# Kernel tuning notes

Measured on AMD Instinct MI355X. Metric: run time of the kernel, lower is better.

Reference implementation:

```python
import jax, jax.numpy as jnp
import numpy as np

DIM = 512
H = 8
HEAD = DIM // H
SCALE = HEAD ** -0.5
B, XL, KL = 4, 1024, 256


def _split(t):
    b, n, _ = t.shape
    return t.reshape(b, n, H, HEAD).transpose(0, 2, 1, 3)


def _merge(t):
    b, h, n, d = t.shape
    return t.transpose(0, 2, 1, 3).reshape(b, n, h * d)


def _qkv(t, W):
    q, k, v = jnp.split(t @ W, 3, axis=-1)
    return _split(q), _split(k), _split(v)


def setup_inputs() -> dict:
    key = jax.random.key(0)
    ks = jax.random.split(key, 20)
    def n(i, shape):
        return jax.random.normal(ks[i], shape, dtype=jnp.float32)
    return {
        "x": n(0, (B, XL, DIM)),
        "kernal": n(1, (B, KL, DIM)),
        "i_x": n(2, (B, XL, DIM)),
        "i_kernal": n(3, (B, KL, DIM)),
        "rd": jax.random.randint(ks[4], (B, KL, XL), 0, 66),
        "polar_pos": jax.random.randint(ks[5], (B, KL, XL), 0, 8),
        "att_mask": jax.random.bernoulli(ks[6], 0.1, (B, H, XL, KL)),
        "i_att_mask": jax.random.bernoulli(ks[7], 0.1, (B, H, XL, KL)),
        "cross_att_mask": jax.random.bernoulli(ks[8], 0.1, (B, H, XL, KL)),
        "Wqkv": n(9, (DIM, 3 * DIM)) * 0.02,
        "Wqkv_i": n(10, (DIM, 3 * DIM)) * 0.02,
        "Wqkv_i2": n(11, (DIM, 3 * DIM)) * 0.02,
        "Wproj": n(12, (DIM, DIM)) * 0.02,
        "bproj": jnp.zeros((DIM,), jnp.float32),
        "Wproj_i": n(13, (DIM, DIM)) * 0.02,
        "bproj_i": jnp.zeros((DIM,), jnp.float32),
        "Wproj_i2": n(14, (DIM, DIM)) * 0.02,
        "bproj_i2": jnp.zeros((DIM,), jnp.float32),
        "dis_embed": n(15, (66, H)) * 0.02,
        "polar_emb": n(16, (8, 1)) * 0.02,
    }


def reference(x, kernal, i_x, i_kernal, rd, polar_pos, att_mask, i_att_mask, cross_att_mask, Wqkv, Wqkv_i, Wqkv_i2, Wproj, bproj, Wproj_i, bproj_i, Wproj_i2, bproj_i2, dis_embed, polar_emb):
    q, k, v = _qkv(x, Wqkv)
    k_q, k_k, k_v = _qkv(kernal, Wqkv)
    i_q, i_k, i_v = _qkv(i_x, Wqkv_i)
    i_k_q, i_k_k, i_k_v = _qkv(i_kernal, Wqkv_i)

    rd_bias = dis_embed[rd].transpose(0, 3, 1, 2)              # [b,h,kl,xl]
    k_x_attn = jnp.einsum('bhkd,bhxd->bhkx', k_q, k) * SCALE   # [b,h,kl,xl]

    # main-orientation: per (b,h,k) sum of |attn| over x grouped by polar bin
    polar = jnp.clip(polar_pos, 0, 7)[:, None, :, :]           # [b,1,kl,xl]
    abs_attn = jnp.abs(k_x_attn)
    ori_sum = jnp.stack([jnp.sum(abs_attn * (polar == o), axis=-1) for o in range(8)], axis=-1)  # [b,h,kl,8]
    main_ori = jnp.argmax(ori_sum, axis=-1)                    # [b,h,kl]
    new_polar = polar - main_ori[..., None]
    new_polar = jnp.where(new_polar < 0, new_polar + 8, new_polar)
    polar_bias = polar_emb[new_polar, 0]                       # [b,h,kl,xl]

    kx = jnp.where(jnp.transpose(att_mask, (0, 1, 3, 2)), -1e6, k_x_attn)
    kx = jax.nn.softmax(kx + rd_bias + polar_bias, axis=-1)
    k_out = _merge(jnp.einsum('bhkx,bhxd->bhkd', kx, v)) @ Wproj + bproj

    x_k = jnp.einsum('bhxd,bhkd->bhxk', q, k_k) * SCALE
    x_k = jnp.where(att_mask, -1e9, x_k)
    x_k = jax.nn.softmax(x_k + jnp.transpose(rd_bias + polar_bias, (0, 1, 3, 2)), axis=-1)
    x_out1 = _merge(jnp.einsum('bhxk,bhkd->bhxd', x_k, k_v)) @ Wproj + bproj

    x_ik = jnp.einsum('bhxd,bhkd->bhxk', q, i_k_k) * SCALE
    x_ik = jax.nn.softmax(jnp.where(cross_att_mask, -1e9, x_ik), axis=-1)
    x_out2 = _merge(jnp.einsum('bhxk,bhkd->bhxd', x_ik, i_k_v)) @ Wproj + bproj
    x_out = x_out1 + x_out2

    ik_ix = jnp.einsum('bhkd,bhxd->bhkx', i_k_q, i_k) * SCALE
    ik_ix = jnp.where(jnp.transpose(i_att_mask, (0, 1, 3, 2)), -1e9, ik_ix)
    ik_ix = jax.nn.softmax(ik_ix, axis=-1)
    i_k_out = _merge(jnp.einsum('bhkx,bhxd->bhkd', ik_ix, i_v)) @ Wproj_i + bproj_i

    i_k2_q, i_k2_k, i_k2_v = _qkv(i_k_out, Wqkv_i2)
    ix_ik2 = jnp.einsum('bhxd,bhkd->bhxk', i_q, i_k2_k) * SCALE
    ix_ik2 = jax.nn.softmax(jnp.where(i_att_mask, -1e9, ix_ik2), axis=-1)
    i_x_out = _merge(jnp.einsum('bhxk,bhkd->bhxd', ix_ik2, i_k2_v)) @ Wproj_i2 + bproj_i2

    return (x_out, k_out, i_x_out)
```

## Files before the change

### kernel.cpp

```cpp
#include <hip/hip_runtime.h>
#include <cstddef>
#include <cstdint>

#define BB 4
#define HH 8
#define HEADD 64
#define DIMM 512
#define XLL 1024
#define KLL 256
#define BHH (BB*HH)

typedef __attribute__((ext_vector_type(8))) short bf16x8;
typedef __attribute__((ext_vector_type(8))) unsigned short u16x8;
typedef __attribute__((ext_vector_type(4))) float f32x4;
typedef unsigned short u16;

__device__ __forceinline__ u16 f2b(float f) {
    unsigned int u = __builtin_bit_cast(unsigned int, f);
    u = u + 0x7fffu + ((u >> 16) & 1u);
    return (u16)(u >> 16);
}
__device__ __forceinline__ float b2f(u16 h) {
    unsigned int u = ((unsigned int)h) << 16;
    return __builtin_bit_cast(float, u);
}
__device__ __forceinline__ f32x4 mfma16(bf16x8 a, bf16x8 b, f32x4 c) {
    return __builtin_amdgcn_mfma_f32_16x16x32_bf16(a, b, c, 0, 0, 0);
}
__device__ __forceinline__ float wred_max(float v) {
    #pragma unroll
    for (int o = 1; o < 64; o <<= 1) v = fmaxf(v, __shfl_xor(v, o, 64));
    return v;
}
__device__ __forceinline__ float wred_sum(float v) {
    #pragma unroll
    for (int o = 1; o < 64; o <<= 1) v += __shfl_xor(v, o, 64);
    return v;
}


__global__ __launch_bounds__(256) void prep_all_k(
    const float* __restrict__ s0, const float* __restrict__ s1,
    const float* __restrict__ s2, const float* __restrict__ s3,
    const float* __restrict__ s4, const float* __restrict__ s5,
    u16* __restrict__ d0, u16* __restrict__ d1, u16* __restrict__ d2,
    u16* __restrict__ d3, u16* __restrict__ d4, u16* __restrict__ d5,
    const int* __restrict__ i_att, unsigned char* __restrict__ iattT8,
    u16* __restrict__ iattBF,
    const int* __restrict__ cross, u16* __restrict__ crossBF)
{
    const int id = blockIdx.x;
    if (id < 3072) {
        __shared__ float t[32][33];
        const float* W; u16* Wt; int N, bx, by;
        if (id < 2304) {
            int which = id / 768, local = id - which * 768;
            W = which == 0 ? s0 : (which == 1 ? s1 : s2);
            Wt = which == 0 ? d0 : (which == 1 ? d1 : d2);
            N = 1536; bx = local % 48; by = local / 48;
        } else {
            int which = (id - 2304) / 256, local = (id - 2304) % 256;
            W = which == 0 ? s3 : (which == 1 ? s4 : s5);
            Wt = which == 0 ? d3 : (which == 1 ? d4 : d5);
            N = 512; bx = local % 16; by = local / 16;
        }
        const int K = 512;
        int tx = threadIdx.x & 31, ty = threadIdx.x >> 5;
        #pragma unroll
        for (int r = ty; r < 32; r += 8)
            t[r][tx] = W[(size_t)(by * 32 + r) * N + bx * 32 + tx];
        __syncthreads();
        #pragma unroll
        for (int r = ty; r < 32; r += 8)
            Wt[(size_t)(bx * 32 + r) * K + by * 32 + tx] = f2b(t[tx][r]);
        return;
    }
    const int id2 = id - 3072;
    const int xt = id2 & 31, kt = (id2 >> 5) & 7, z = id2 >> 8;
    const int bh = z & 31;
    const int tid = threadIdx.x;
    const u16 NEG = f2b(-1e9f);
    const int sl = tid >> 7, rem = tid & 127, l = rem >> 1, nilow = rem & 1;
    const int lg = l >> 4, lr_ = l & 15;
    const int xl0 = sl * 16 + lg * 4, kl = nilow * 16 + lr_;
    if (z < 32) {
        __shared__ unsigned char t8[32][33];
        const int tx = tid & 31, ty = tid >> 5;
        #pragma unroll
        for (int r = ty; r < 32; r += 8)
            t8[r][tx] = (unsigned char)(i_att[((size_t)bh * 1024 + xt * 32 + r) * 256 + kt * 32 + tx] != 0);
        __syncthreads();
        #pragma unroll
        for (int r = ty; r < 32; r += 8)
            iattT8[((size_t)bh * 256 + kt * 32 + r) * 1024 + xt * 32 + tx] = t8[tx][r];
        ushort4 o;
        o.x = t8[xl0 + 0][kl] ? NEG : (u16)0;
        o.y = t8[xl0 + 1][kl] ? NEG : (u16)0;
        o.z = t8[xl0 + 2][kl] ? NEG : (u16)0;
        o.w = t8[xl0 + 3][kl] ? NEG : (u16)0;
        size_t eb = (((size_t)bh * 64 + xt * 2 + sl) * 8 + kt) * 512 + (size_t)l * 8 + nilow * 4;
        *reinterpret_cast<ushort4*>(iattBF + eb) = o;
    } else {
        const int kg = kt * 32 + kl;
        u16 o_[4];
        #pragma unroll
        for (int j = 0; j < 4; ++j) {
            int mm = cross[((size_t)bh * 1024 + xt * 32 + xl0 + j) * 256 + kg];
            o_[j] = mm ? NEG : (u16)0;
        }
        ushort4 o; o.x = o_[0]; o.y = o_[1]; o.z = o_[2]; o.w = o_[3];
        size_t eb = (((size_t)bh * 64 + xt * 2 + sl) * 8 + kt) * 512 + (size_t)l * 8 + nilow * 4;
        *reinterpret_cast<ushort4*>(crossBF + eb) = o;
    }
}

__global__ __launch_bounds__(256) void main_ori_k8(
    const u16* __restrict__ S, const int* __restrict__ polar,
    int* __restrict__ MO)
{
    const int blk = blockIdx.x;
    const int b = blk >> 8, k = blk & 255;
    const int tid = threadIdx.x;
    const int wave = tid >> 6, lane = tid & 63;
    const int c = tid * 4;
    int4 p4 = *reinterpret_cast<const int4*>(polar + ((size_t)b * 256 + k) * 1024 + c);
    int pp[4] = { p4.x, p4.y, p4.z, p4.w };
    #pragma unroll
    for (int j = 0; j < 4; ++j) { int p = pp[j]; pp[j] = p < 0 ? 0 : (p > 7 ? 7 : p); }
    __shared__ float sred[4][8];
    for (int h = 0; h < 8; ++h) {
        const int bh = b * 8 + h;
        ushort4 sv = *reinterpret_cast<const ushort4*>(S + ((size_t)bh * 256 + k) * 1024 + c);
        float av[4] = { fabsf(b2f(sv.x)), fabsf(b2f(sv.y)), fabsf(b2f(sv.z)), fabsf(b2f(sv.w)) };
        float bins[8] = {};
        #pragma unroll
        for (int j = 0; j < 4; ++j) {
            #pragma unroll
            for (int o = 0; o < 8; ++o) bins[o] += (pp[j] == o) ? av[j] : 0.0f;
        }
        #pragma unroll
        for (int o = 0; o < 8; ++o) bins[o] = wred_sum(bins[o]);
        if (lane == 0) {
            #pragma unroll
            for (int o = 0; o < 8; ++o) sred[wave][o] = bins[o];
        }
        __syncthreads();
        if (tid == 0) {
            int best = 0; float bv = -1.0f;
            #pragma unroll
            for (int o = 0; o < 8; ++o) {
                float s = sred[0][o] + sred[1][o] + sred[2][o] + sred[3][o];
                if (s > bv) { bv = s; best = o; }
            }
            MO[bh * 256 + k] = best;
        }
        __syncthreads();
    }
}

__global__ __launch_bounds__(256) void bias_build_k(
    const int* __restrict__ rd, const int* __restrict__ polar,
    const int* __restrict__ att, const float* __restrict__ dis,
    const float* __restrict__ pemb, const int* __restrict__ MO,
    u16* __restrict__ biasF, u16* __restrict__ bias1)
{
    const int b = blockIdx.z;
    const int xt = blockIdx.x * 32, kt = blockIdx.y * 32;
    const int tid = threadIdx.x;
    __shared__ float dsh[528];
    __shared__ int rds[32][33];
    __shared__ int pls[32][33];
    __shared__ u16 bt[32][33];
    for (int i = tid; i < 528; i += 256) dsh[i] = dis[i];
    const int tx = tid & 31, ty = tid >> 5;
    #pragma unroll
    for (int r = ty; r < 32; r += 8) {
        size_t src = ((size_t)b * 256 + kt + r) * 1024 + xt + tx;
        rds[tx][r] = rd[src];
        int p = polar[src]; pls[tx][r] = p < 0 ? 0 : (p > 7 ? 7 : p);
    }
    float pe[8];
    #pragma unroll
    for (int o = 0; o < 8; ++o) pe[o] = pemb[o];
    __syncthreads();
    const int sl = tid >> 7, rem = tid & 127, l = rem >> 1, nilow = rem & 1;
    const int lg = l >> 4, lr_ = l & 15;
    const int xl0 = sl * 16 + lg * 4, kl = nilow * 16 + lr_;
    const int kg = kt + kl;
    const u16 NEG9 = f2b(-1e9f), NEG6 = f2b(-1e6f);
    for (int h = 0; h < 8; ++h) {
        const int bh = b * 8 + h;
        int mo = MO[bh * 256 + kg];
        u16 o9[4];
        #pragma unroll
        for (int j = 0; j < 4; ++j) {
            int xl = xl0 + j;
            int mm = att[((size_t)bh * 1024 + xt + xl) * 256 + kg];
            float v = dsh[rds[xl][kl] * 8 + h] + pe[(pls[xl][kl] - mo + 8) & 7];
            u16 vb = f2b(v);
            o9[j] = mm ? NEG9 : vb;
            bt[xl][kl] = mm ? NEG6 : vb;
        }
        size_t eb = (((size_t)bh * 64 + (xt >> 4) + sl) * 8 + (kt >> 5)) * 512 + (size_t)l * 8 + nilow * 4;
        ushort4 ov; ov.x = o9[0]; ov.y = o9[1]; ov.z = o9[2]; ov.w = o9[3];
        *reinterpret_cast<ushort4*>(biasF + eb) = ov;
        __syncthreads();
        const int k_ = tid >> 3, x4 = (tid & 7) * 4;
        ushort4 o2;
        o2.x = bt[x4 + 0][k_]; o2.y = bt[x4 + 1][k_];
        o2.z = bt[x4 + 2][k_]; o2.w = bt[x4 + 3][k_];
        *reinterpret_cast<ushort4*>(bias1 + ((size_t)bh * 256 + kt + k_) * 1024 + xt + x4) = o2;
        __syncthreads();
    }
}

template<typename AT>
__device__ __forceinline__ void gemm_core_128(
    const AT* __restrict__ A, const AT* __restrict__ A2,
    const u16* __restrict__ Wt,
    int rb, int cb, short* Asl, short* Bsl, f32x4 (&acc)[4][4])
{
    constexpr bool F32 = sizeof(AT) == 4;
    const int tid = threadIdx.x;
    const int w = tid >> 6, lane = tid & 63;
    const int lr = lane & 15, lk = (lane >> 4) * 8;
    const int wr = (w >> 1) * 64, wc = (w & 1) * 64;
    const int srow = tid >> 3, skc = (tid & 7) * 8;
    const AT* gA = A + (size_t)(rb + srow) * 512 + skc;
    const AT* gA2 = A2 ? A2 + (size_t)(rb + srow) * 512 + skc : nullptr;
    const u16* gB = Wt + (size_t)(cb + srow) * 512 + skc;
    float4 ral[4], rah[4];
    bf16x8 rab[4], rab2[4], rw[4];
    #pragma unroll
    for (int it = 0; it < 4; ++it) {
        if constexpr (F32) {
            ral[it] = *reinterpret_cast<const float4*>(gA + (size_t)it * 32 * 512);
            rah[it] = *reinterpret_cast<const float4*>(gA + (size_t)it * 32 * 512 + 4);
        } else {
            rab[it] = *reinterpret_cast<const bf16x8*>(gA + (size_t)it * 32 * 512);
            if (gA2) rab2[it] = *reinterpret_cast<const bf16x8*>(gA2 + (size_t)it * 32 * 512);
        }
        rw[it] = *reinterpret_cast<const bf16x8*>(gB + (size_t)it * 32 * 512);
    }
    for (int t = 0; t < 8; ++t) {
        #pragma unroll
        for (int it = 0; it < 4; ++it) {
            if constexpr (F32) {
                u16x8 o;
                o[0] = f2b(ral[it].x); o[1] = f2b(ral[it].y);
                o[2] = f2b(ral[it].z); o[3] = f2b(ral[it].w);
                o[4] = f2b(rah[it].x); o[5] = f2b(rah[it].y);
                o[6] = f2b(rah[it].z); o[7] = f2b(rah[it].w);
                *reinterpret_cast<u16x8*>(&Asl[(it * 32 + srow) * 72 + skc]) = o;
            } else {
                if (gA2) {
                    u16x8 o;
                    #pragma unroll
                    for (int e = 0; e < 8; ++e)
                        o[e] = f2b(b2f((u16)rab[it][e]) + b2f((u16)rab2[it][e]));
                    *reinterpret_cast<u16x8*>(&Asl[(it * 32 + srow) * 72 + skc]) = o;
                } else {
                    *reinterpret_cast<bf16x8*>(&Asl[(it * 32 + srow) * 72 + skc]) = rab[it];
                }
            }
            *reinterpret_cast<bf16x8*>(&Bsl[(it * 32 + srow) * 72 + skc]) = rw[it];
        }
        if (t < 7) {
            const int k0 = (t + 1) * 64;
            #pragma unroll
            for (int it = 0; it < 4; ++it) {
                if constexpr (F32) {
                    ral[it] = *reinterpret_cast<const float4*>(gA + k0 + (size_t)it * 32 * 512);
                    rah[it] = *reinterpret_cast<const float4*>(gA + k0 + (size_t)it * 32 * 512 + 4);
                } else {
                    rab[it] = *reinterpret_cast<const bf16x8*>(gA + k0 + (size_t)it * 32 * 512);
                    if (gA2) rab2[it] = *reinterpret_cast<const bf16x8*>(gA2 + k0 + (size_t)it * 32 * 512);
                }
                rw[it] = *reinterpret_cast<const bf16x8*>(gB + k0 + (size_t)it * 32 * 512);
            }
        }
        __syncthreads();
        #pragma unroll
        for (int ks = 0; ks < 2; ++ks) {
            bf16x8 af[4], bf_[4];
            #pragma unroll
            for (int mi = 0; mi < 4; ++mi)
                af[mi] = *reinterpret_cast<const bf16x8*>(&Asl[(wr + mi * 16 + lr) * 72 + ks * 32 + lk]);
            #pragma unroll
            for (int ni = 0; ni < 4; ++ni)
                bf_[ni] = *reinterpret_cast<const bf16x8*>(&Bsl[(wc + ni * 16 + lr) * 72 + ks * 32 + lk]);
            #pragma unroll
            for (int mi = 0; mi < 4; ++mi)
                #pragma unroll
                for (int ni = 0; ni < 4; ++ni)
                    acc[mi][ni] = mfma16(af[mi], bf_[ni], acc[mi][ni]);
        }
        __syncthreads();
    }
}

template<typename AT>
__device__ __forceinline__ void qkv_body(
    const AT* __restrict__ A, const u16* __restrict__ Wt,
    u16* __restrict__ qb, u16* __restrict__ kb, u16* __restrict__ vt,
    int sl, int rb, int cb)
{
    __shared__ __align__(16) short Ls[2 * 128 * 72];
    short* Asl = Ls;
    short* Bsl = Ls + 128 * 72;
    f32x4 acc[4][4] = {};
    gemm_core_128<AT>(A, nullptr, Wt, rb, cb, Asl, Bsl, acc);
    const int tid = threadIdx.x;
    const int wave = tid >> 6, lane = tid & 63;
    const int lr = lane & 15, lg = lane >> 4;
    const int wr = (wave >> 1) * 64, wc = (wave & 1) * 64;
    const int seq = 1 << sl, smask = seq - 1;
    if (cb < 1024) {
        const float scl = (cb < 512) ? 0.125f : 1.0f;
        #pragma unroll
        for (int mi = 0; mi < 4; ++mi)
            #pragma unroll
            for (int ni = 0; ni < 4; ++ni) {
                int row = wr + mi * 16 + lg * 4;
                int col = wc + ni * 16 + lr;
                f32x4 v = acc[mi][ni];
                #pragma unroll
                for (int j = 0; j < 4; ++j)
                    Ls[(row + j) * 136 + col] = (short)f2b(v[j] * scl);
            }
        __syncthreads();
        u16* dst = (cb < 512) ? qb : kb;
        if (dst) {
            const int cbase = (cb < 512) ? cb : cb - 512;
            #pragma unroll
            for (int p = 0; p < 8; ++p) {
                int slot = p * 256 + tid;
                int row = slot >> 4;
                int half = (slot >> 3) & 1;
                int inner = slot & 7;
                int m = rb + row;
                int bb = m >> sl, n = m & smask;
                int cg = cbase + half * 64;
                int h = cg >> 6;
                u16x8 val = *reinterpret_cast<u16x8*>(&Ls[row * 136 + half * 64 + inner * 8]);
                *reinterpret_cast<u16x8*>(
                    &dst[(((size_t)bb * HH + h) * seq + n) * 64 + inner * 8]) = val;
            }
        }
    } else {
        #pragma unroll
        for (int mi = 0; mi < 4; ++mi)
            #pragma unroll
            for (int ni = 0; ni < 4; ++ni) {
                int col = wc + ni * 16 + lr;
                int row0 = wr + mi * 16 + lg * 4;
                f32x4 v = acc[mi][ni];
                #pragma unroll
                for (int j = 0; j < 4; ++j)
                    Ls[col * 136 + row0 + j] = (short)f2b(v[j]);
            }
        __syncthreads();
        const int bb = rb >> sl, n0 = rb & smask;
        #pragma unroll
        for (int p = 0; p < 4; ++p) {
            int slot = p * 256 + tid;
            int col = slot >> 3;
            int inner = slot & 7;
            int dg = (cb - 1024) + col;
            int h = dg >> 6, d = dg & 63;
            u16* vrow = vt + ((((size_t)bb * HH + h) * 64 + d) << sl) + n0;
            u16x8 v0 = *reinterpret_cast<u16x8*>(&Ls[col * 136 + inner * 8]);
            u16x8 v1 = *reinterpret_cast<u16x8*>(&Ls[col * 136 + 64 + inner * 8]);
            *reinterpret_cast<u16x8*>(vrow + inner * 8) = v0;
            *reinterpret_cast<u16x8*>(vrow + 64 + inner * 8) = v1;
        }
    }
}

__global__ __launch_bounds__(256, 3) void gemm_qkv_all_k(
    const float* __restrict__ A0, const float* __restrict__ A1,
    const float* __restrict__ A2, const float* __restrict__ A3,
    const u16* __restrict__ W01, const u16* __restrict__ W23,
    u16* q0, u16* k0, u16* v0, u16* q1, u16* k1, u16* v1,
    u16* q2, u16* k2, u16* v2, u16* q3, u16* k3, u16* v3)
{
    const int lin = blockIdx.x;
    const int swz = (lin & 7) * 120 + (lin >> 3);
    const int x = swz % 12, y = swz / 12;
    const float* A; const u16* Wt; u16 *qb, *kb, *vt; int sl, ry;
    if (y < 32)      { A = A0; Wt = W01; qb = q0; kb = k0; vt = v0; sl = 10; ry = y; }
    else if (y < 40) { A = A1; Wt = W01; qb = q1; kb = k1; vt = v1; sl = 8;  ry = y - 32; }
    else if (y < 72) { A = A2; Wt = W23; qb = q2; kb = k2; vt = v2; sl = 10; ry = y - 40; }
    else             { A = A3; Wt = W23; qb = q3; kb = k3; vt = v3; sl = 8;  ry = y - 72; }
    qkv_body<float>(A, Wt, qb, kb, vt, sl, ry * 128, x * 128);
}

__global__ __launch_bounds__(256, 3) void gemm_qkv2_k(
    const u16* __restrict__ A, const u16* __restrict__ Wt,
    u16* kb, u16* vt)
{
    qkv_body<u16>(A, Wt, nullptr, kb, vt, 8, blockIdx.y * 128, (blockIdx.x + 4) * 128);
}

template<bool OUTBF>
__device__ __forceinline__ void proj_body(
    const u16* __restrict__ A, const u16* __restrict__ A2,
    const u16* __restrict__ Wt,
    const float* __restrict__ bias, float bscale, void* __restrict__ outp,
    int rb, int cb)
{
    __shared__ __align__(16) short Ls[2 * 128 * 72];
    f32x4 acc[4][4] = {};
    gemm_core_128<u16>(A, A2, Wt, rb, cb, Ls, Ls + 128 * 72, acc);
    const int tid = threadIdx.x;
    const int wave = tid >> 6, lane = tid & 63;
    const int lr = lane & 15;
    const int wr = (wave >> 1) * 64, wc = (wave & 1) * 64;
    #pragma unroll
    for (int mi = 0; mi < 4; ++mi) {
        int m0 = rb + wr + mi * 16 + (lane >> 4) * 4;
        #pragma unroll
        for (int ni = 0; ni < 4; ++ni) {
            int c = cb + wc + ni * 16 + lr;
            float bv = bscale * bias[c];
            f32x4 v = acc[mi][ni];
            #pragma unroll
            for (int j = 0; j < 4; ++j) {
                size_t o = (size_t)(m0 + j) * 512 + c;
                if (OUTBF) reinterpret_cast<u16*>(outp)[o] = f2b(v[j] + bv);
                else       reinterpret_cast<float*>(outp)[o] = v[j] + bv;
            }
        }
    }
}

__global__ __launch_bounds__(256, 3) void gemm_proj_bf16_k(
    const u16* __restrict__ A, const u16* __restrict__ Wt,
    const float* __restrict__ bias, float bscale, u16* __restrict__ outp)
{
    proj_body<true>(A, nullptr, Wt, bias, bscale, outp, blockIdx.y * 128, blockIdx.x * 128);
}

__global__ __launch_bounds__(256, 3) void gemm_proj3_k(
    const u16* __restrict__ A0, const u16* __restrict__ A0b,
    const u16* __restrict__ A1, const u16* __restrict__ A2,
    const u16* __restrict__ W, const u16* __restrict__ Wi2,
    const float* __restrict__ bp, const float* __restrict__ bpi2,
    float* __restrict__ o0, float* __restrict__ o1, float* __restrict__ o2)
{
    const int id = blockIdx.x;
    const u16 *A, *Ax; const u16* Wt; const float* bias; float bscale; float* outp; int x, y;
    if (id < 128)      { A = A0; Ax = A0b; Wt = W;   bias = bp;   bscale = 2.0f; outp = o0; x = id & 3; y = id >> 2; }
    else if (id < 256) { A = A1; Ax = nullptr; Wt = Wi2; bias = bpi2; bscale = 1.0f; outp = o1; x = (id - 128) & 3; y = (id - 128) >> 2; }
    else               { A = A2; Ax = nullptr; Wt = W;   bias = bp;   bscale = 1.0f; outp = o2; x = (id - 256) & 3; y = (id - 256) >> 2; }
    proj_body<false>(A, Ax, Wt, bias, bscale, outp, y * 128, x * 128);
}

__global__ __launch_bounds__(256, 4) void scores_pair_k(
    const u16* __restrict__ A1, const u16* __restrict__ B1, u16* __restrict__ S1,
    const u16* __restrict__ A2, const u16* __restrict__ B2, u16* __restrict__ S2)
{
    __shared__ __align__(16) short Ls[2 * 128 * 72];
    short* As = Ls;
    short* Bs = Ls + 128 * 72;
    const int z = blockIdx.z, bh = z & 31;
    const u16* Aq = (z < 32) ? A1 : A2;
    const u16* Bk = (z < 32) ? B1 : B2;
    u16* S = (z < 32) ? S1 : S2;
    const int tid = threadIdx.x;
    const int wave = tid >> 6, lane = tid & 63;
    const int lr = lane & 15, lg = lane >> 4, lk = lg * 8;
    const int rb = blockIdx.y * 128, cb = blockIdx.x * 128;
    const int wr = (wave >> 1) * 64, wc = (wave & 1) * 64;
    const u16* Ap = Aq + (size_t)bh * 256 * 64;
    const u16* Bp = Bk + (size_t)bh * 1024 * 64;
    const int srow = tid >> 3, skc = (tid & 7) * 8;
    #pragma unroll
    for (int it = 0; it < 4; ++it) {
        int row = it * 32 + srow;
        *reinterpret_cast<bf16x8*>(&As[row * 72 + skc]) =
            *reinterpret_cast<const bf16x8*>(Ap + (size_t)(rb + row) * 64 + skc);
        *reinterpret_cast<bf16x8*>(&Bs[row * 72 + skc]) =
            *reinterpret_cast<const bf16x8*>(Bp + (size_t)(cb + row) * 64 + skc);
    }
    __syncthreads();
    f32x4 acc[4][4] = {};
    #pragma unroll
    for (int ks = 0; ks < 2; ++ks) {
        bf16x8 af[4], bf_[4];
        #pragma unroll
        for (int mi = 0; mi < 4; ++mi)
            af[mi] = *reinterpret_cast<const bf16x8*>(&As[(wr + mi * 16 + lr) * 72 + ks * 32 + lk]);
        #pragma unroll
        for (int ni = 0; ni < 4; ++ni)
            bf_[ni] = *reinterpret_cast<const bf16x8*>(&Bs[(wc + ni * 16 + lr) * 72 + ks * 32 + lk]);
        #pragma unroll
        for (int mi = 0; mi < 4; ++mi)
            #pragma unroll
            for (int ni = 0; ni < 4; ++ni)
                acc[mi][ni] = mfma16(af[mi], bf_[ni], acc[mi][ni]);
    }
    __syncthreads();
    #pragma unroll
    for (int mi = 0; mi < 4; ++mi)
        #pragma unroll
        for (int ni = 0; ni < 4; ++ni) {
            int row = wr + mi * 16 + lg * 4;
            int col = wc + ni * 16 + lr;
            f32x4 v = acc[mi][ni];
            #pragma unroll
            for (int j = 0; j < 4; ++j)
                Ls[(row + j) * 136 + col] = (short)f2b(v[j]);
        }
    __syncthreads();
    #pragma unroll
    for (int p = 0; p < 8; ++p) {
        int slot = p * 256 + tid;
        int row = slot >> 4;
        int chunk = slot & 15;
        u16x8 val = *reinterpret_cast<u16x8*>(&Ls[row * 136 + chunk * 8]);
        *reinterpret_cast<u16x8*>(
            &S[((size_t)bh * 256 + rb + row) * 1024 + cb + chunk * 8]) = val;
    }
}

__global__ __launch_bounds__(256) void softmax_pair_k(
    u16* __restrict__ S1, const u16* __restrict__ bias1,
    u16* __restrict__ S2, const unsigned char* __restrict__ maskT)
{
    const int rg = blockIdx.x;
    const bool first = rg < 8192;
    const int row_g = first ? rg : rg - 8192;
    const int tid = threadIdx.x;
    const int wave = tid >> 6, lane = tid & 63;
    const int c = tid * 4;
    u16* rowp = (first ? S1 : S2) + (size_t)row_g * 1024;
    ushort4 sv = *reinterpret_cast<const ushort4*>(rowp + c);
    float s[4] = { b2f(sv.x), b2f(sv.y), b2f(sv.z), b2f(sv.w) };
    if (first) {
        ushort4 bv = *reinterpret_cast<const ushort4*>(bias1 + (size_t)row_g * 1024 + c);
        s[0] += b2f(bv.x); s[1] += b2f(bv.y); s[2] += b2f(bv.z); s[3] += b2f(bv.w);
    } else {
        uchar4 mk = *reinterpret_cast<const uchar4*>(maskT + (size_t)row_g * 1024 + c);
        if (mk.x) s[0] = -1e9f; if (mk.y) s[1] = -1e9f;
        if (mk.z) s[2] = -1e9f; if (mk.w) s[3] = -1e9f;
    }
    __shared__ float swv[4];
    float lm = fmaxf(fmaxf(s[0], s[1]), fmaxf(s[2], s[3]));
    lm = wred_max(lm);
    if (lane == 0) swv[wave] = lm;
    __syncthreads();
    float m = fmaxf(fmaxf(swv[0], swv[1]), fmaxf(swv[2], swv[3]));
    __syncthreads();
    float ls = 0.0f;
    #pragma unroll
    for (int j = 0; j < 4; ++j) { s[j] = __expf(s[j] - m); ls += s[j]; }
    ls = wred_sum(ls);
    if (lane == 0) swv[wave] = ls;
    __syncthreads();
    float inv = 1.0f / (swv[0] + swv[1] + swv[2] + swv[3]);
    ushort4 ov = { f2b(s[0] * inv), f2b(s[1] * inv), f2b(s[2] * inv), f2b(s[3] * inv) };
    *reinterpret_cast<ushort4*>(rowp + c) = ov;
}

__global__ __launch_bounds__(256, 4) void pv_pair_k(
    const u16* __restrict__ P1, const u16* __restrict__ V1, u16* __restrict__ o1,
    const u16* __restrict__ P2, const u16* __restrict__ V2, u16* __restrict__ o2)
{
    __shared__ __align__(16) short Ps[4 * 16 * 72];
    const int z = blockIdx.z;
    const u16* P = z ? P2 : P1;
    const u16* V = z ? V2 : V1;
    u16* out = z ? o2 : o1;
    const int tid = threadIdx.x;
    const int wave = tid >> 6, lane = tid & 63;
    const int lr = lane & 15, lg = lane >> 4, lk = lg * 8;
    const int bh = blockIdx.y, b = bh >> 3, h = bh & 7;
    const int rb = blockIdx.x * 64;
    const int wr = wave * 16;
    f32x4 acc[4] = {};
    const u16* Pb = P + ((size_t)bh * 256 + rb) * 1024;
    const u16* Vb = V + (size_t)bh * 64 * 1024;
    for (int c0 = 0; c0 < 1024; c0 += 64) {
        #pragma unroll
        for (int ks = 0; ks < 2; ++ks) {
            bf16x8 ap = *reinterpret_cast<const bf16x8*>(
                Pb + (size_t)(wr + lr) * 1024 + c0 + ks * 32 + lk);
            #pragma unroll
            for (int ni = 0; ni < 4; ++ni) {
                bf16x8 vv = *reinterpret_cast<const bf16x8*>(
                    Vb + (size_t)(ni * 16 + lr) * 1024 + c0 + ks * 32 + lk);
                acc[ni] = mfma16(ap, vv, acc[ni]);
            }
        }
    }
    short* myP = &Ps[wave * 16 * 72];
    #pragma unroll
    for (int ni = 0; ni < 4; ++ni) {
        int d = ni * 16 + lr;
        f32x4 v = acc[ni];
        #pragma unroll
        for (int j = 0; j < 4; ++j)
            myP[(lg * 4 + j) * 72 + d] = (short)f2b(v[j]);
    }
    #pragma unroll
    for (int p = 0; p < 2; ++p) {
        int slot = p * 64 + lane;
        int rloc = slot >> 3;
        int inner = slot & 7;
        int r0 = rb + wr + rloc;
        u16x8 val = *reinterpret_cast<u16x8*>(&myP[rloc * 72 + inner * 8]);
        *reinterpret_cast<u16x8*>(
            &out[((size_t)(b * 256 + r0)) * 512 + h * 64 + inner * 8]) = val;
    }
}

__global__ __launch_bounds__(256, 4) void attn_all_k(
    const u16* __restrict__ Q0, const u16* __restrict__ IQ0,
    const u16* __restrict__ K1, const u16* __restrict__ V1t,
    const u16* __restrict__ B1F, u16* __restrict__ out1,
    const u16* __restrict__ K2, const u16* __restrict__ V2t,
    const u16* __restrict__ B2F, u16* __restrict__ out2,
    const u16* __restrict__ K3, const u16* __restrict__ V3t,
    const u16* __restrict__ B3F, u16* __restrict__ out3)
{
    const int tid = threadIdx.x;
    const int w = tid >> 6, lane = tid & 63;
    const int lr = lane & 15, lg = lane >> 4, lk = lg * 8;
    int lin = blockIdx.x;
    const u16 *Qp, *Kp, *Vp, *BF; u16* outm;
    if (lin < 512)        { Qp = Q0;  Kp = K1; Vp = V1t; BF = B1F; outm = out1; }
    else if (lin < 1024)  { Qp = Q0;  Kp = K2; Vp = V2t; BF = B2F; outm = out2; lin -= 512; }
    else                  { Qp = IQ0; Kp = K3; Vp = V3t; BF = B3F; outm = out3; lin -= 1024; }
    const int xcd = lin & 7, idx = lin >> 3;
    const int bh = xcd * 4 + (idx & 3);
    const int rb = (idx >> 2) * 64;
    const int b = bh >> 3, h = bh & 7;
    const int wr = w * 16;
    const int strip = (rb >> 4) + w;

    __shared__ __align__(16) short Ps[4 * 16 * 264];
    short* myP = &Ps[w * 16 * 264];

    bf16x8 qf0, qf1;
    {
        const u16* Qb = Qp + ((size_t)bh * 1024 + rb + wr + lr) * 64;
        qf0 = *reinterpret_cast<const bf16x8*>(Qb + lk);
        qf1 = *reinterpret_cast<const bf16x8*>(Qb + 32 + lk);
    }

    bf16x8 breg[8];
    {
        const u16* bb = BF + (((size_t)bh * 64 + strip) * 8) * 512 + (size_t)lane * 8;
        #pragma unroll
        for (int itp = 0; itp < 8; ++itp)
            breg[itp] = *reinterpret_cast<const bf16x8*>(bb + (size_t)itp * 512);
    }
    const u16* Kb = Kp + (size_t)bh * 256 * 64;
    f32x4 acc[16];
    #pragma unroll
    for (int ni = 0; ni < 16; ++ni) acc[ni] = (f32x4){0.f, 0.f, 0.f, 0.f};
    #pragma unroll
    for (int ni = 0; ni < 16; ++ni) {
        bf16x8 b0 = *reinterpret_cast<const bf16x8*>(Kb + (size_t)(ni * 16 + lr) * 64 + lk);
        acc[ni] = mfma16(qf0, b0, acc[ni]);
    }
    #pragma unroll
    for (int ni = 0; ni < 16; ++ni) {
        bf16x8 b1 = *reinterpret_cast<const bf16x8*>(Kb + (size_t)(ni * 16 + lr) * 64 + 32 + lk);
        acc[ni] = mfma16(qf1, b1, acc[ni]);
    }
    float mx[4] = { -3.4e38f, -3.4e38f, -3.4e38f, -3.4e38f };
    #pragma unroll
    for (int ni = 0; ni < 16; ++ni) {
        const bf16x8 br = breg[ni >> 1];
        #pragma unroll
        for (int j = 0; j < 4; ++j) {
            float v = acc[ni][j] + b2f((u16)br[(ni & 1) * 4 + j]);
            acc[ni][j] = v;
            mx[j] = fmaxf(mx[j], v);
        }
    }
    #pragma unroll
    for (int j = 0; j < 4; ++j) {
        #pragma unroll
        for (int o = 1; o < 16; o <<= 1) mx[j] = fmaxf(mx[j], __shfl_xor(mx[j], o, 64));
    }
    float sm[4] = {};
    #pragma unroll
    for (int ni = 0; ni < 16; ++ni) {
        #pragma unroll
        for (int j = 0; j < 4; ++j) {
            float e = __expf(acc[ni][j] - mx[j]);
            acc[ni][j] = e;
            sm[j] += e;
        }
    }
    #pragma unroll
    for (int j = 0; j < 4; ++j) {
        #pragma unroll
        for (int o = 1; o < 16; o <<= 1) sm[j] += __shfl_xor(sm[j], o, 64);
        sm[j] = 1.0f / sm[j];
    }
    #pragma unroll
    for (int ni = 0; ni < 16; ++ni)
        #pragma unroll
        for (int j = 0; j < 4; ++j)
            myP[(lg * 4 + j) * 264 + ni * 16 + lr] = (short)f2b(acc[ni][j] * sm[j]);
    f32x4 acc2[4] = {};
    #pragma unroll
    for (int kc = 0; kc < 8; ++kc) {
        bf16x8 ap = *reinterpret_cast<const bf16x8*>(&myP[lr * 264 + kc * 32 + lk]);
        #pragma unroll
        for (int ni = 0; ni < 4; ++ni) {
            bf16x8 vv = *reinterpret_cast<const bf16x8*>(
                Vp + ((size_t)bh * 64 + ni * 16 + lr) * 256 + kc * 32 + lk);
            acc2[ni] = mfma16(ap, vv, acc2[ni]);
        }
    }
    #pragma unroll
    for (int ni = 0; ni < 4; ++ni) {
        int d = ni * 16 + lr;
        f32x4 v = acc2[ni];
        #pragma unroll
        for (int j = 0; j < 4; ++j)
            myP[(lg * 4 + j) * 72 + d] = (short)f2b(v[j]);
    }
    #pragma unroll
    for (int p = 0; p < 2; ++p) {
        int slot = p * 64 + lane;
        int rloc = slot >> 3;
        int inner = slot & 7;
        int row = rb + wr + rloc;
        u16x8 val = *reinterpret_cast<u16x8*>(&myP[rloc * 72 + inner * 8]);
        *reinterpret_cast<u16x8*>(
            &outm[((size_t)(b * 1024 + row)) * 512 + h * 64 + inner * 8]) = val;
    }
}

extern "C" void kernel_launch(void* const* d_in, const int* in_sizes, int n_in,
                              void* d_out, int out_size, void* d_ws, size_t ws_size,
                              hipStream_t stream)
{
    const float* x        = (const float*)d_in[0];
    const float* kernal   = (const float*)d_in[1];
    const float* i_x      = (const float*)d_in[2];
    const float* i_kernal = (const float*)d_in[3];
    const int*   rd       = (const int*)d_in[4];
    const int*   polar    = (const int*)d_in[5];
    const int*   att      = (const int*)d_in[6];
    const int*   i_att    = (const int*)d_in[7];
    const int*   cross    = (const int*)d_in[8];
    const float* Wqkv     = (const float*)d_in[9];
    const float* Wqkv_i   = (const float*)d_in[10];
    const float* Wqkv_i2  = (const float*)d_in[11];
    const float* Wproj    = (const float*)d_in[12];
    const float* bproj    = (const float*)d_in[13];
    const float* Wproj_i  = (const float*)d_in[14];
    const float* bproj_i  = (const float*)d_in[15];
    const float* Wproj_i2 = (const float*)d_in[16];
    const float* bproj_i2 = (const float*)d_in[17];
    const float* dis      = (const float*)d_in[18];
    const float* pemb     = (const float*)d_in[19];

    float* out = (float*)d_out;
    float* x_out   = out;
    float* k_out   = out + (size_t)BB * XLL * DIMM;
    float* i_x_out = k_out + (size_t)BB * KLL * DIMM;

    char* ws = (char*)d_ws;
    size_t off = 0;
    auto alloc = [&](size_t bytes) { void* p = ws + off; off += (bytes + 255) & ~(size_t)255; return p; };

    const size_t NAX = (size_t)BB * XLL * DIMM;
    const size_t NAK = (size_t)BB * KLL * DIMM;
    const size_t NHX = (size_t)BHH * XLL * HEADD;
    const size_t NHK = (size_t)BHH * KLL * HEADD;
    const size_t NS  = (size_t)BHH * KLL * XLL;

    u16* WqkvT    = (u16*)alloc((size_t)1536 * 512 * 2);
    u16* WqkvIT   = (u16*)alloc((size_t)1536 * 512 * 2);
    u16* WqkvI2T  = (u16*)alloc((size_t)1536 * 512 * 2);
    u16* WprojT   = (u16*)alloc((size_t)512 * 512 * 2);
    u16* WprojIT  = (u16*)alloc((size_t)512 * 512 * 2);
    u16* WprojI2T = (u16*)alloc((size_t)512 * 512 * 2);
    u16* Q    = (u16*)alloc(NHX * 2);
    u16* KX   = (u16*)alloc(NHX * 2);
    u16* VXt  = (u16*)alloc(NHX * 2);
    u16* IQ   = (u16*)alloc(NHX * 2);
    u16* IK   = (u16*)alloc(NHX * 2);
    u16* IVt  = (u16*)alloc(NHX * 2);
    u16* KQ   = (u16*)alloc(NHK * 2);
    u16* KK   = (u16*)alloc(NHK * 2);
    u16* KVt  = (u16*)alloc(NHK * 2);
    u16* IKQ  = (u16*)alloc(NHK * 2);
    u16* IKK  = (u16*)alloc(NHK * 2);
    u16* IKVt = (u16*)alloc(NHK * 2);
    u16* K2K  = (u16*)alloc(NHK * 2);
    u16* K2Vt = (u16*)alloc(NHK * 2);
    u16* SPa  = (u16*)alloc(NS * 2);
    u16* SPb  = (u16*)alloc(NS * 2);
    u16* KMb  = (u16*)alloc(NAK * 2);
    u16* KMb2 = (u16*)alloc(NAK * 2);
    u16* XMb  = (u16*)alloc(NAX * 2);
    u16* XMb2 = (u16*)alloc(NAX * 2);
    u16* XMc  = (u16*)alloc(NAX * 2);
    u16* IKOUTb = (u16*)alloc(NAK * 2);
    u16* biasF = (u16*)alloc(NS * 2);
    u16* bias1 = (u16*)alloc(NS * 2);
    u16* crossBF = (u16*)alloc(NS * 2);
    u16* iattBF  = (u16*)alloc(NS * 2);
    unsigned char* iattT8 = (unsigned char*)alloc(NS);
    int* MO   = (int*)alloc((size_t)BHH * KLL * 4);

    dim3 blk(256);

    prep_all_k<<<dim3(19456), blk, 0, stream>>>(
        Wqkv, Wqkv_i, Wqkv_i2, Wproj, Wproj_i, Wproj_i2,
        WqkvT, WqkvIT, WqkvI2T, WprojT, WprojIT, WprojI2T,
        i_att, iattT8, iattBF, cross, crossBF);

    gemm_qkv_all_k<<<dim3(960), blk, 0, stream>>>(
        x, kernal, i_x, i_kernal, WqkvT, WqkvIT,
        Q, KX, VXt, KQ, KK, KVt, IQ, IK, IVt, IKQ, IKK, IKVt);

    scores_pair_k<<<dim3(8, 2, 64), blk, 0, stream>>>(KQ, KX, SPa, IKQ, IK, SPb);
    main_ori_k8<<<dim3(BB * KLL), blk, 0, stream>>>(SPa, polar, MO);
    bias_build_k<<<dim3(32, 8, BB), blk, 0, stream>>>(rd, polar, att, dis, pemb, MO, biasF, bias1);
    softmax_pair_k<<<dim3(16384), blk, 0, stream>>>(SPa, bias1, SPb, iattT8);
    pv_pair_k<<<dim3(4, 32, 2), blk, 0, stream>>>(SPa, VXt, KMb, SPb, IVt, KMb2);
    gemm_proj_bf16_k<<<dim3(4, 8), blk, 0, stream>>>(KMb2, WprojIT, bproj_i, 1.0f, IKOUTb);
    gemm_qkv2_k<<<dim3(8, 8), blk, 0, stream>>>(IKOUTb, WqkvI2T, K2K, K2Vt);
    attn_all_k<<<dim3(1536), blk, 0, stream>>>(
        Q, IQ, KK, KVt, biasF, XMb, IKK, IKVt, crossBF, XMc,
        K2K, K2Vt, iattBF, XMb2);
    gemm_proj3_k<<<dim3(288), blk, 0, stream>>>(
        XMb, XMc, XMb2, KMb, WprojT, WprojI2T, bproj, bproj_i2, x_out, i_x_out, k_out);

    (void)in_sizes; (void)n_in; (void)out_size; (void)ws_size;
}
```

Before: 256.9 us.

## Fuse row softmax into PV matmul kernel for kernel-query attention pair

Removes the separate softmax_pair_k pass and computes each row's softmax inside the PV kernel. A first pass over the score row finds the max. A second pass builds the exponentials on the fly, feeds them to the MFMA, and normalises the accumulator at the end. This avoids writing the normalised probabilities back to global memory and drops one kernel launch. In exchange it reads the score, bias and mask rows twice, and the PV grid has only 256 blocks, so the softmax work now runs at much lower parallelism.

```diff
diff --git a/kernel.cpp b/kernel.cpp
--- a/kernel.cpp
+++ b/kernel.cpp
@@ -14,6 +14,7 @@
 typedef __attribute__((ext_vector_type(8))) unsigned short u16x8;
 typedef __attribute__((ext_vector_type(4))) float f32x4;
 typedef unsigned short u16;
+typedef unsigned long long u64;
 
 __device__ __forceinline__ u16 f2b(float f) {
     unsigned int u = __builtin_bit_cast(unsigned int, f);
@@ -524,76 +525,89 @@
     }
 }
 
-__global__ __launch_bounds__(256) void softmax_pair_k(
-    u16* __restrict__ S1, const u16* __restrict__ bias1,
-    u16* __restrict__ S2, const unsigned char* __restrict__ maskT)
-{
-    const int rg = blockIdx.x;
-    const bool first = rg < 8192;
-    const int row_g = first ? rg : rg - 8192;
-    const int tid = threadIdx.x;
-    const int wave = tid >> 6, lane = tid & 63;
-    const int c = tid * 4;
-    u16* rowp = (first ? S1 : S2) + (size_t)row_g * 1024;
-    ushort4 sv = *reinterpret_cast<const ushort4*>(rowp + c);
-    float s[4] = { b2f(sv.x), b2f(sv.y), b2f(sv.z), b2f(sv.w) };
-    if (first) {
-        ushort4 bv = *reinterpret_cast<const ushort4*>(bias1 + (size_t)row_g * 1024 + c);
-        s[0] += b2f(bv.x); s[1] += b2f(bv.y); s[2] += b2f(bv.z); s[3] += b2f(bv.w);
-    } else {
-        uchar4 mk = *reinterpret_cast<const uchar4*>(maskT + (size_t)row_g * 1024 + c);
-        if (mk.x) s[0] = -1e9f; if (mk.y) s[1] = -1e9f;
-        if (mk.z) s[2] = -1e9f; if (mk.w) s[3] = -1e9f;
-    }
-    __shared__ float swv[4];
-    float lm = fmaxf(fmaxf(s[0], s[1]), fmaxf(s[2], s[3]));
-    lm = wred_max(lm);
-    if (lane == 0) swv[wave] = lm;
-    __syncthreads();
-    float m = fmaxf(fmaxf(swv[0], swv[1]), fmaxf(swv[2], swv[3]));
-    __syncthreads();
-    float ls = 0.0f;
-    #pragma unroll
-    for (int j = 0; j < 4; ++j) { s[j] = __expf(s[j] - m); ls += s[j]; }
-    ls = wred_sum(ls);
-    if (lane == 0) swv[wave] = ls;
-    __syncthreads();
-    float inv = 1.0f / (swv[0] + swv[1] + swv[2] + swv[3]);
-    ushort4 ov = { f2b(s[0] * inv), f2b(s[1] * inv), f2b(s[2] * inv), f2b(s[3] * inv) };
-    *reinterpret_cast<ushort4*>(rowp + c) = ov;
-}
-
-__global__ __launch_bounds__(256, 4) void pv_pair_k(
-    const u16* __restrict__ P1, const u16* __restrict__ V1, u16* __restrict__ o1,
-    const u16* __restrict__ P2, const u16* __restrict__ V2, u16* __restrict__ o2)
-{
-    __shared__ __align__(16) short Ps[4 * 16 * 72];
-    const int z = blockIdx.z;
-    const u16* P = z ? P2 : P1;
-    const u16* V = z ? V2 : V1;
-    u16* out = z ? o2 : o1;
+template<bool HASB>
+__device__ __forceinline__ void pv_fused_body(
+    const u16* __restrict__ P, const u16* __restrict__ BIAS,
+    const unsigned char* __restrict__ MSK,
+    const u16* __restrict__ V, u16* __restrict__ out, short* Ps)
+{
     const int tid = threadIdx.x;
     const int wave = tid >> 6, lane = tid & 63;
     const int lr = lane & 15, lg = lane >> 4, lk = lg * 8;
     const int bh = blockIdx.y, b = bh >> 3, h = bh & 7;
     const int rb = blockIdx.x * 64;
     const int wr = wave * 16;
+    const size_t rowg = (size_t)bh * 256 + rb + wr + lr;
+    const u16* Prow = P + rowg * 1024;
+    const u16* Brow = HASB ? BIAS + rowg * 1024 : nullptr;
+    const unsigned char* Mrow = HASB ? nullptr : MSK + rowg * 1024;
+    const u16* Vb = V + (size_t)bh * 64 * 1024;
+
+    float m = -3.4e38f;
+    for (int c0 = 0; c0 < 1024; c0 += 64) {
+        #pragma unroll
+        for (int ks = 0; ks < 2; ++ks) {
+            const int cc = c0 + ks * 32 + lk;
+            bf16x8 sv = *reinterpret_cast<const bf16x8*>(Prow + cc);
+            if (HASB) {
+                bf16x8 bv = *reinterpret_cast<const bf16x8*>(Brow + cc);
+                #pragma unroll
+                for (int e = 0; e < 8; ++e)
+                    m = fmaxf(m, b2f((u16)sv[e]) + b2f((u16)bv[e]));
+            } else {
+                u64 mk = *reinterpret_cast<const u64*>(Mrow + cc);
+                #pragma unroll
+                for (int e = 0; e < 8; ++e) {
+                    float s = ((mk >> (e * 8)) & 0xFFull) ? -1e9f : b2f((u16)sv[e]);
+                    m = fmaxf(m, s);
+                }
+            }
+        }
+    }
+    m = fmaxf(m, __shfl_xor(m, 16, 64));
+    m = fmaxf(m, __shfl_xor(m, 32, 64));
+
     f32x4 acc[4] = {};
-    const u16* Pb = P + ((size_t)bh * 256 + rb) * 1024;
-    const u16* Vb = V + (size_t)bh * 64 * 1024;
+    float sum = 0.0f;
     for (int c0 = 0; c0 < 1024; c0 += 64) {
         #pragma unroll
         for (int ks = 0; ks < 2; ++ks) {
-            bf16x8 ap = *reinterpret_cast<const bf16x8*>(
-                Pb + (size_t)(wr + lr) * 1024 + c0 + ks * 32 + lk);
+            const int cc = c0 + ks * 32 + lk;
+            bf16x8 sv = *reinterpret_cast<const bf16x8*>(Prow + cc);
+            bf16x8 ap;
+            if (HASB) {
+                bf16x8 bv = *reinterpret_cast<const bf16x8*>(Brow + cc);
+                #pragma unroll
+                for (int e = 0; e < 8; ++e) {
+                    float ev = __expf(b2f((u16)sv[e]) + b2f((u16)bv[e]) - m);
+                    sum += ev;
+                    ap[e] = (short)f2b(ev);
+                }
+            } else {
+                u64 mk = *reinterpret_cast<const u64*>(Mrow + cc);
+                #pragma unroll
+                for (int e = 0; e < 8; ++e) {
+                    float s = ((mk >> (e * 8)) & 0xFFull) ? -1e9f : b2f((u16)sv[e]);
+                    float ev = __expf(s - m);
+                    sum += ev;
+                    ap[e] = (short)f2b(ev);
+                }
+            }
             #pragma unroll
             for (int ni = 0; ni < 4; ++ni) {
                 bf16x8 vv = *reinterpret_cast<const bf16x8*>(
-                    Vb + (size_t)(ni * 16 + lr) * 1024 + c0 + ks * 32 + lk);
+                    Vb + (size_t)(ni * 16 + lr) * 1024 + cc);
                 acc[ni] = mfma16(ap, vv, acc[ni]);
             }
         }
     }
+    sum += __shfl_xor(sum, 16, 64);
+    sum += __shfl_xor(sum, 32, 64);
+    const float inv = 1.0f / sum;
+    float invj[4];
+    #pragma unroll
+    for (int j = 0; j < 4; ++j) invj[j] = __shfl(inv, lg * 4 + j, 64);
+
     short* myP = &Ps[wave * 16 * 72];
     #pragma unroll
     for (int ni = 0; ni < 4; ++ni) {
@@ -601,7 +615,7 @@
         f32x4 v = acc[ni];
         #pragma unroll
         for (int j = 0; j < 4; ++j)
-            myP[(lg * 4 + j) * 72 + d] = (short)f2b(v[j]);
+            myP[(lg * 4 + j) * 72 + d] = (short)f2b(v[j] * invj[j]);
     }
     #pragma unroll
     for (int p = 0; p < 2; ++p) {
@@ -613,6 +627,19 @@
         *reinterpret_cast<u16x8*>(
             &out[((size_t)(b * 256 + r0)) * 512 + h * 64 + inner * 8]) = val;
     }
+}
+
+__global__ __launch_bounds__(256, 4) void pv_fused_k(
+    const u16* __restrict__ P1, const u16* __restrict__ B1,
+    const u16* __restrict__ V1, u16* __restrict__ o1,
+    const u16* __restrict__ P2, const unsigned char* __restrict__ M2,
+    const u16* __restrict__ V2, u16* __restrict__ o2)
+{
+    __shared__ __align__(16) short Ps[4 * 16 * 72];
+    if (blockIdx.z == 0)
+        pv_fused_body<true>(P1, B1, nullptr, V1, o1, Ps);
+    else
+        pv_fused_body<false>(P2, nullptr, M2, V2, o2, Ps);
 }
 
 __global__ __launch_bounds__(256, 4) void attn_all_k(
@@ -827,8 +854,8 @@
     scores_pair_k<<<dim3(8, 2, 64), blk, 0, stream>>>(KQ, KX, SPa, IKQ, IK, SPb);
     main_ori_k8<<<dim3(BB * KLL), blk, 0, stream>>>(SPa, polar, MO);
     bias_build_k<<<dim3(32, 8, BB), blk, 0, stream>>>(rd, polar, att, dis, pemb, MO, biasF, bias1);
-    softmax_pair_k<<<dim3(16384), blk, 0, stream>>>(SPa, bias1, SPb, iattT8);
-    pv_pair_k<<<dim3(4, 32, 2), blk, 0, stream>>>(SPa, VXt, KMb, SPb, IVt, KMb2);
+    pv_fused_k<<<dim3(4, 32, 2), blk, 0, stream>>>(
+        SPa, bias1, VXt, KMb, SPb, iattT8, IVt, KMb2);
     gemm_proj_bf16_k<<<dim3(4, 8), blk, 0, stream>>>(KMb2, WprojIT, bproj_i, 1.0f, IKOUTb);
     gemm_qkv2_k<<<dim3(8, 8), blk, 0, stream>>>(IKOUTb, WqkvI2T, K2K, K2Vt);
     attn_all_k<<<dim3(1536), blk, 0, stream>>>(
```

After: 249.9 us (median of 2 runs). 2.7% less time.
